# Optimization experiments

Measured on AMD Instinct MI355X. Metric: run time of the kernel, lower is better.

## Reference

```python
import jax, jax.numpy as jnp
import numpy as np

B, C, N = 8, 512, 2048

def setup_inputs() -> dict:
    key = jax.random.key(0)
    ks = jax.random.split(key, 7)
    s = 1.0 / np.sqrt(C)
    return {
        "x": jax.random.normal(ks[0], (B, C, N), dtype=jnp.float32),
        "wq": jax.random.normal(ks[1], (C, C), dtype=jnp.float32) * s,
        "bq": jax.random.normal(ks[2], (C,), dtype=jnp.float32) * s,
        "wk": jax.random.normal(ks[3], (C, C), dtype=jnp.float32) * s,
        "bk": jax.random.normal(ks[4], (C,), dtype=jnp.float32) * s,
        "wv": jax.random.normal(ks[5], (C, C), dtype=jnp.float32) * s,
        "bv": jax.random.normal(ks[6], (C,), dtype=jnp.float32) * s,
    }

def reference(x, wq, bq, wk, bk, wv, bv):
    # Conv1d with kernel=1 == pointwise channel matmul: [B,C,N] -> [B,C,N]
    q = jnp.einsum('oc,bcn->bon', wq, x) + bq[None, :, None]
    k = jnp.einsum('oc,bcn->bon', wk, x) + bk[None, :, None]
    v = jnp.einsum('oc,bcn->bon', wv, x) + bv[None, :, None]
    # scores[b,i,j] = sum_c q[b,c,i] * k[b,c,j]; softmax over j (no scaling, as in source)
    scores = jnp.einsum('bci,bcj->bij', q, k)
    attn = jax.nn.softmax(scores, axis=-1)  # [B,N,N]
    # out[b,c,i] = sum_j v[b,c,j] * attn[b,i,j]
    out = jnp.einsum('bcj,bij->bci', v, attn)
    return out + x
```

## Files before the change

### kernel.cpp

```cpp
#include <hip/hip_runtime.h>
#include <hip/hip_bf16.h>

typedef _Float16 half_t;
typedef _Float16 f16x8 __attribute__((ext_vector_type(8)));
typedef float f32x4 __attribute__((ext_vector_type(4)));

#define AS1 __attribute__((address_space(1)))
#define AS3 __attribute__((address_space(3)))

constexpr int CB = 512;
constexpr int NB = 2048;
constexpr int BB = 8;

__device__ inline f32x4 mfma16(f16x8 a, f16x8 b, f32x4 c) {
  return __builtin_amdgcn_mfma_f32_16x16x32_f16(a, b, c, 0, 0, 0);
}

__device__ inline void xcd_swizzle(int& bx, int& by, int& bz) {
  const int gx = gridDim.x, gy = gridDim.y, gz = gridDim.z;
  const int nwg = gx * gy * gz;
  int lin = blockIdx.x + gx * (blockIdx.y + gy * blockIdx.z);
  if ((nwg & 7) == 0) {
    const int q = nwg >> 3;
    lin = (lin & 7) * q + (lin >> 3);
  }
  bx = lin % gx;
  int tmp = lin / gx;
  by = tmp % gy;
  bz = tmp / gy;
}

__global__ __launch_bounds__(256) void prep_all(
    const float* __restrict__ x, const float* __restrict__ wq,
    const float* __restrict__ wk, const float* __restrict__ wv,
    const float* __restrict__ bq,
    half_t* __restrict__ xh, half_t* __restrict__ xn,
    half_t* __restrict__ wvh, float* __restrict__ u, float* __restrict__ Gp) {
  __shared__ float smem[64 * 68 * 2];
  const int b = blockIdx.x;
  const int t = threadIdx.x;

  if (b < 8192) {
    float (*tile)[33] = (float(*)[33])smem;
    const int bz = b >> 10, by = (b >> 6) & 15, bx = b & 63;
    const int c0 = by * 32, n0 = bx * 32;
    const int tx = t & 31, ty = t >> 5;
    const float* xb = x + (size_t)bz * CB * NB;
    half_t* xnb = xn + (size_t)bz * CB * NB;
#pragma unroll
    for (int r = 0; r < 4; r++) {
      float v = xb[(size_t)(c0 + ty + 8 * r) * NB + n0 + tx];
      tile[ty + 8 * r][tx] = v;
      xnb[(size_t)(c0 + ty + 8 * r) * NB + n0 + tx] = (half_t)v;
    }
    __syncthreads();
    size_t base = (size_t)bz * NB * CB;
#pragma unroll
    for (int r = 0; r < 4; r++)
      xh[base + (size_t)(n0 + ty + 8 * r) * CB + c0 + tx] = (half_t)tile[tx][ty + 8 * r];
  } else if (b < 8704) {
    const int g = b - 8192;
    const int d0 = (g & 7) * 64, c0 = ((g >> 3) & 7) * 64, o0 = (g >> 6) * 64;
    float (*aq)[68] = (float(*)[68])smem;
    float (*ak)[68] = (float(*)[68])(smem + 64 * 68);
    {
      const int r = t >> 2, cbase = (t & 3) * 16;
      const float* q = wq + (size_t)(o0 + r) * CB + c0 + cbase;
      const float* k = wk + (size_t)(o0 + r) * CB + d0 + cbase;
#pragma unroll
      for (int q4 = 0; q4 < 4; q4++) {
        *(float4*)&aq[r][cbase + q4 * 4] = *(const float4*)(q + q4 * 4);
        *(float4*)&ak[r][cbase + q4 * 4] = *(const float4*)(k + q4 * 4);
      }
    }
    __syncthreads();
    const int tc = t & 15, td = t >> 4;
    float acc[4][4] = {};
#pragma unroll 8
    for (int o = 0; o < 64; o++) {
      float4 a4 = *(const float4*)&aq[o][tc * 4];
      float4 b4 = *(const float4*)&ak[o][td * 4];
      float av[4] = {a4.x, a4.y, a4.z, a4.w};
      float bv[4] = {b4.x, b4.y, b4.z, b4.w};
#pragma unroll
      for (int i = 0; i < 4; i++)
#pragma unroll
        for (int j = 0; j < 4; j++)
          acc[i][j] += av[i] * bv[j];
    }
    float* gz = Gp + (size_t)(g >> 6) * CB * CB;
#pragma unroll
    for (int i = 0; i < 4; i++) {
      int c = c0 + tc * 4 + i;
#pragma unroll
      for (int j = 0; j < 4; j++)
        gz[(size_t)c * CB + d0 + td * 4 + j] = acc[i][j];
    }
  } else {
    const int p = b - 8704;
    if (p < 1024) {
      int i = p * 256 + t;
      if (i < CB * CB) wvh[i] = (half_t)wv[i];
    } else {
      int d = (p - 1024) * 256 + t;
      if (d < CB) {
        float s = 0.0f;
        for (int o = 0; o < CB; o++) s += bq[o] * wk[(size_t)o * CB + d];
        u[d] = s;
      }
    }
  }
}

__global__ __launch_bounds__(256) void prep2(
    const float* __restrict__ Gp, half_t* __restrict__ Gh,
    const half_t* __restrict__ xh, const float* __restrict__ u,
    float* __restrict__ ub) {
  const int b = blockIdx.x;
  const int t = threadIdx.x;
  if (b < 1024) {
    int i = b * 256 + t;
    if (i < CB * CB) {
      float s = 0.0f;
#pragma unroll
      for (int z = 0; z < 8; z++) s += Gp[(size_t)z * CB * CB + i];
      Gh[i] = (half_t)s;
    }
  } else {
    __shared__ float us[CB];
    for (int i = t; i < CB; i += 256) us[i] = u[i];
    __syncthreads();
    int row = (b - 1024) * 4 + (t >> 6);
    int lane = t & 63;
    f16x8 vh = *(const f16x8*)(xh + (size_t)row * CB + lane * 8);
    float s = 0.0f;
#pragma unroll
    for (int i = 0; i < 8; i++) s += us[lane * 8 + i] * (float)vh[i];
#pragma unroll
    for (int off = 32; off; off >>= 1) s += __shfl_xor(s, off);
    if (lane == 0) ub[row] = s;
  }
}

__global__ __launch_bounds__(512) void gemm_s256(
    const half_t* __restrict__ xh, const half_t* __restrict__ YTh,
    short* __restrict__ Ss, const float* __restrict__ ub) {
  constexpr int NT = 16;
  constexpr int BUFE = 16384;
  __shared__ alignas(16) half_t sm[3 * BUFE];

  int bxi, byi, bzi;
  xcd_swizzle(bxi, byi, bzi);
  const int t = threadIdx.x;
  const int z = bzi;
  const half_t* Ap = xh  + (size_t)z * NB * CB + (size_t)(byi * 256) * CB;
  const half_t* Bp = YTh + (size_t)z * NB * CB + (size_t)(bxi * 256) * CB;

  const int wid = t >> 6, wm = wid >> 2, wn = wid & 3;
  const int l15 = t & 15, hi = (t >> 4) & 3;
  const int sr = t >> 2, sc = (t & 3) * 8;

  f32x4 acc[8][4] = {};

  auto stageA = [&](int buf, int kt) {
    half_t* dst = sm + buf * BUFE;
#pragma unroll
    for (int i = 0; i < 2; i++)
      __builtin_amdgcn_global_load_lds(
          (const AS1 void*)(Ap + (size_t)(i * 128 + sr) * CB + kt * 32 + sc),
          (AS3 void*)(dst + i * 4096 + t * 8), 16, 0, 0);
  };
  auto stageB = [&](int buf, int kt) {
    half_t* dst = sm + buf * BUFE + 8192;
#pragma unroll
    for (int i = 0; i < 2; i++)
      __builtin_amdgcn_global_load_lds(
          (const AS1 void*)(Bp + (size_t)(i * 128 + sr) * CB + kt * 32 + sc),
          (AS3 void*)(dst + i * 4096 + t * 8), 16, 0, 0);
  };

  stageA(0, 0); stageB(0, 0);
  stageA(1, 1); stageB(1, 1);
  asm volatile("s_waitcnt vmcnt(4)" ::: "memory");
  __builtin_amdgcn_s_barrier();
  asm volatile("" ::: "memory");

  int rb = 0;
  for (int kt = 0; kt < NT; kt++) {
    const half_t* Abuf = sm + rb * BUFE;
    const half_t* Bbuf = Abuf + 8192;
    const int sb = (rb + 2 >= 3) ? rb - 1 : rb + 2;

    f16x8 af[8], bf[4];
#pragma unroll
    for (int f = 0; f < 4; f++)
      af[f] = *(const f16x8*)(Abuf + (wm * 128 + f * 16 + l15) * 32 + hi * 8);
#pragma unroll
    for (int n = 0; n < 4; n++)
      bf[n] = *(const f16x8*)(Bbuf + (wn * 64 + n * 16 + l15) * 32 + hi * 8);
    if (kt + 2 < NT) stageA(sb, kt + 2);
    __builtin_amdgcn_s_barrier();
    asm volatile("s_waitcnt lgkmcnt(0)" ::: "memory");
    __builtin_amdgcn_s_setprio(1);
#pragma unroll
    for (int m = 0; m < 4; m++)
#pragma unroll
      for (int n = 0; n < 4; n++)
        acc[m][n] = mfma16(af[m], bf[n], acc[m][n]);
    __builtin_amdgcn_s_setprio(0);
    __builtin_amdgcn_s_barrier();
    asm volatile("" ::: "memory");

#pragma unroll
    for (int f = 4; f < 8; f++)
      af[f] = *(const f16x8*)(Abuf + (wm * 128 + f * 16 + l15) * 32 + hi * 8);
    if (kt + 2 < NT) stageB(sb, kt + 2);
    __builtin_amdgcn_s_barrier();
    asm volatile("s_waitcnt lgkmcnt(0)" ::: "memory");
    __builtin_amdgcn_s_setprio(1);
#pragma unroll
    for (int m = 4; m < 8; m++)
#pragma unroll
      for (int n = 0; n < 4; n++)
        acc[m][n] = mfma16(af[m], bf[n], acc[m][n]);
    __builtin_amdgcn_s_setprio(0);
    if (kt + 1 < NT) {
      if (kt + 2 < NT) asm volatile("s_waitcnt vmcnt(4)" ::: "memory");
      else             asm volatile("s_waitcnt vmcnt(0)" ::: "memory");
    }
    __builtin_amdgcn_s_barrier();
    asm volatile("" ::: "memory");
    rb = (rb + 1 == 3) ? 0 : rb + 1;
  }

  const int row0 = byi * 256 + wm * 128;
  const int col0 = bxi * 256 + wn * 64;
  short* Sz = Ss + (size_t)z * NB * NB;
  const float* ubz = ub + (size_t)z * NB;
#pragma unroll
  for (int m = 0; m < 8; m++) {
    int rowb = row0 + m * 16 + hi * 4;
#pragma unroll
    for (int n = 0; n < 4; n++) {
      int col = col0 + n * 16 + l15;
      float bc = ubz[col];
#pragma unroll
      for (int r = 0; r < 4; r++) {
        float sv = fminf(fmaxf((acc[m][n][r] + bc) * 256.0f, -32767.0f), 32767.0f);
        Sz[(size_t)(rowb + r) * NB + col] = (short)__float2int_rn(sv);
      }
    }
  }
}

template <int BIAS, int EPI, int NT>
__global__ __launch_bounds__(256) void gemm_nt(
    const half_t* __restrict__ A, int lda, long sA,
    const half_t* __restrict__ Bh, int ldb, long sB,
    void* __restrict__ D, int ldd, long sD,
    const float* __restrict__ bias, long sBias,
    const half_t* __restrict__ R, int ldr, long sR) {
  constexpr int TSZ = 128 * 32;
  __shared__ alignas(16) half_t sm[2 * 2 * TSZ];

  int bxi, byi, bzi;
  xcd_swizzle(bxi, byi, bzi);
  const int t = threadIdx.x;
  const int z = bzi;
  const half_t* Ab  = A  + (size_t)z * sA + (size_t)(byi * 128) * lda;
  const half_t* Bbh = Bh + (size_t)z * sB + (size_t)(bxi * 128) * ldb;
  const int wid = t >> 6, l15 = t & 15, hi = (t >> 4) & 3;
  const int wr = wid >> 1, wc = wid & 1;
  const int lineA = t >> 2, eoff = (t & 3) * 8;

  f32x4 acc[4][4] = {};

  auto stage = [&](int buf, int kt) {
    half_t* base = sm + buf * (2 * TSZ);
#pragma unroll
    for (int p = 0; p < 2; p++) {
      size_t goA = (size_t)(p * 64 + lineA) * lda + kt * 32 + eoff;
      size_t goB = (size_t)(p * 64 + lineA) * ldb + kt * 32 + eoff;
      int lo = p * 2048 + t * 8;
      __builtin_amdgcn_global_load_lds((const AS1 void*)(Ab + goA),  (AS3 void*)(base + lo), 16, 0, 0);
      __builtin_amdgcn_global_load_lds((const AS1 void*)(Bbh + goB), (AS3 void*)(base + TSZ + lo), 16, 0, 0);
    }
  };

  stage(0, 0);
  __syncthreads();
  int cur = 0;
  for (int kt = 0; kt < NT; kt++) {
    if (kt + 1 < NT) stage(cur ^ 1, kt + 1);
    const half_t* bb = sm + cur * (2 * TSZ);
    f16x8 af[4], bf[4];
#pragma unroll
    for (int f = 0; f < 4; f++) {
      af[f] = *(const f16x8*)(bb + (wr * 64 + f * 16 + l15) * 32 + hi * 8);
      bf[f] = *(const f16x8*)(bb + TSZ + (wc * 64 + f * 16 + l15) * 32 + hi * 8);
    }
#pragma unroll
    for (int fm = 0; fm < 4; fm++)
#pragma unroll
      for (int fn = 0; fn < 4; fn++)
        acc[fm][fn] = mfma16(af[fm], bf[fn], acc[fm][fn]);
    __syncthreads();
    cur ^= 1;
  }

  const int row0 = byi * 128 + wr * 64;
  const int col0 = bxi * 128 + wc * 64;
#pragma unroll
  for (int fm = 0; fm < 4; fm++) {
    int rowb = row0 + fm * 16 + hi * 4;
#pragma unroll
    for (int fn = 0; fn < 4; fn++) {
      int col = col0 + fn * 16 + l15;
      float bc = (BIAS == 1) ? bias[(size_t)z * sBias + col] : 0.0f;
#pragma unroll
      for (int r = 0; r < 4; r++) {
        float val = acc[fm][fn][r] + bc;
        size_t di = (size_t)(rowb + r) * ldd + col;
        if (EPI == 3) {
          val += (float)R[(size_t)z * sR + (size_t)(rowb + r) * ldr + col];
          ((float*)D)[(size_t)z * sD + di] = val;
        } else {
          float sv = fminf(fmaxf(val * 256.0f, -32767.0f), 32767.0f);
          ((short*)D)[(size_t)z * sD + di] = (short)__float2int_rn(sv);
        }
      }
    }
  }
}

__global__ __launch_bounds__(256) void gemm_vyt(
    const half_t* __restrict__ xh, const half_t* __restrict__ wvh,
    const half_t* __restrict__ Gh, const float* __restrict__ bv,
    half_t* __restrict__ v, half_t* __restrict__ YTh) {
  constexpr int TSZ = 128 * 32;
  __shared__ alignas(16) half_t sm[2 * 2 * TSZ];

  int bxi, byi, bzi;
  xcd_swizzle(bxi, byi, bzi);
  const int t = threadIdx.x;

  const half_t* Ab;
  const half_t* Bb;
  half_t* Dz;
  int ldd, row0b, col0b;
  const float* rowbias = nullptr;
  if (bzi < 8) {
    const int z = bzi;
    Ab = wvh + (size_t)(byi * 128) * CB;
    Bb = xh + (size_t)z * NB * CB + (size_t)(bxi * 128) * CB;
    Dz = v + (size_t)z * CB * NB;
    ldd = NB; row0b = byi * 128; col0b = bxi * 128;
    rowbias = bv;
  } else {
    const int z = bzi - 8;
    const int lin2 = byi * 16 + bxi;
    const int xp = lin2 & 3, yp = lin2 >> 2;
    Ab = xh + (size_t)z * NB * CB + (size_t)(yp * 128) * CB;
    Bb = Gh + (size_t)(xp * 128) * CB;
    Dz = YTh + (size_t)z * NB * CB;
    ldd = CB; row0b = yp * 128; col0b = xp * 128;
  }

  const int wid = t >> 6, l15 = t & 15, hi = (t >> 4) & 3;
  const int wr = wid >> 1, wc = wid & 1;
  const int lineA = t >> 2, eoff = (t & 3) * 8;

  f32x4 acc[4][4] = {};

  auto stage = [&](int buf, int kt) {
    half_t* base = sm + buf * (2 * TSZ);
#pragma unroll
    for (int p = 0; p < 2; p++) {
      size_t go = (size_t)(p * 64 + lineA) * CB + kt * 32 + eoff;
      int lo = p * 2048 + t * 8;
      __builtin_amdgcn_global_load_lds((const AS1 void*)(Ab + go), (AS3 void*)(base + lo), 16, 0, 0);
      __builtin_amdgcn_global_load_lds((const AS1 void*)(Bb + go), (AS3 void*)(base + TSZ + lo), 16, 0, 0);
    }
  };

  stage(0, 0);
  __syncthreads();
  int cur = 0;
  for (int kt = 0; kt < 16; kt++) {
    if (kt + 1 < 16) stage(cur ^ 1, kt + 1);
    const half_t* bb = sm + cur * (2 * TSZ);
    f16x8 af[4], bf[4];
#pragma unroll
    for (int f = 0; f < 4; f++) {
      af[f] = *(const f16x8*)(bb + (wr * 64 + f * 16 + l15) * 32 + hi * 8);
      bf[f] = *(const f16x8*)(bb + TSZ + (wc * 64 + f * 16 + l15) * 32 + hi * 8);
    }
#pragma unroll
    for (int fm = 0; fm < 4; fm++)
#pragma unroll
      for (int fn = 0; fn < 4; fn++)
        acc[fm][fn] = mfma16(af[fm], bf[fn], acc[fm][fn]);
    __syncthreads();
    cur ^= 1;
  }

  const int row0 = row0b + wr * 64;
  const int col0 = col0b + wc * 64;
#pragma unroll
  for (int fm = 0; fm < 4; fm++) {
    int rowb = row0 + fm * 16 + hi * 4;
#pragma unroll
    for (int fn = 0; fn < 4; fn++) {
      int col = col0 + fn * 16 + l15;
#pragma unroll
      for (int r = 0; r < 4; r++) {
        float val = acc[fm][fn][r];
        if (rowbias) val += rowbias[rowb + r];
        Dz[(size_t)(rowb + r) * ldd + col] = (half_t)val;
      }
    }
  }
}

struct alignas(16) H8 { half_t h[8]; };
struct alignas(16) S8 { short s[8]; };

__global__ __launch_bounds__(256) void softmax_rows(const short* __restrict__ S,
                                                    half_t* __restrict__ P) {
  const short* row = S + (size_t)blockIdx.x * NB;
  int t = threadIdx.x;
  S8 r8 = *reinterpret_cast<const S8*>(row + t * 8);
  float vals[8];
#pragma unroll
  for (int i = 0; i < 8; i++) vals[i] = (float)r8.s[i] * 0.00390625f;
  float m = vals[0];
#pragma unroll
  for (int i = 1; i < 8; i++) m = fmaxf(m, vals[i]);
#pragma unroll
  for (int off = 32; off; off >>= 1) m = fmaxf(m, __shfl_xor(m, off));
  __shared__ float redm[4], reds[4];
  if ((t & 63) == 0) redm[t >> 6] = m;
  __syncthreads();
  m = fmaxf(fmaxf(redm[0], redm[1]), fmaxf(redm[2], redm[3]));
  float e[8], s = 0.0f;
#pragma unroll
  for (int i = 0; i < 8; i++) { e[i] = __expf(vals[i] - m); s += e[i]; }
#pragma unroll
  for (int off = 32; off; off >>= 1) s += __shfl_xor(s, off);
  if ((t & 63) == 0) reds[t >> 6] = s;
  __syncthreads();
  s = reds[0] + reds[1] + reds[2] + reds[3];
  float inv = 1.0f / s;
  H8 ob;
#pragma unroll
  for (int i = 0; i < 8; i++) ob.h[i] = (half_t)(e[i] * inv);
  *reinterpret_cast<H8*>(P + (size_t)blockIdx.x * NB + t * 8) = ob;
}

extern "C" void kernel_launch(void* const* d_in, const int* in_sizes, int n_in,
                              void* d_out, int out_size, void* d_ws, size_t ws_size,
                              hipStream_t stream) {
  const float* x  = (const float*)d_in[0];
  const float* wq = (const float*)d_in[1];
  const float* bq = (const float*)d_in[2];
  const float* wk = (const float*)d_in[3];
  const float* wv = (const float*)d_in[5];
  const float* bv = (const float*)d_in[6];
  float* out = (float*)d_out;

  const size_t MB = 1u << 20;
  if (ws_size < 196 * MB) return;

  char* ws = (char*)d_ws;
  half_t* xh   = (half_t*)(ws + 0);
  half_t* YTh  = (half_t*)(ws + 16 * MB);
  half_t* v    = (half_t*)(ws + 32 * MB);
  short*  Ss   = (short*)(ws + 48 * MB);
  float*  Gp   = (float*)(ws + 48 * MB);
  half_t* Pd   = (half_t*)(ws + 112 * MB);
  half_t* xn   = (half_t*)(ws + 176 * MB);
  half_t* Gh   = (half_t*)(ws + 192 * MB);
  half_t* wvh  = (half_t*)(ws + 192 * MB + 512 * 1024);
  float*  u    = (float*)(ws + 193 * MB);
  float*  ub   = (float*)(ws + 193 * MB + 256 * 1024);

  prep_all<<<9730, 256, 0, stream>>>(x, wq, wk, wv, bq, xh, xn, wvh, u, Gp);
  prep2<<<5120, 256, 0, stream>>>(Gp, Gh, xh, u, ub);

  gemm_vyt<<<dim3(16, 4, 16), 256, 0, stream>>>(xh, wvh, Gh, bv, v, YTh);

  gemm_s256<<<dim3(8, 8, 8), 512, 0, stream>>>(xh, YTh, Ss, ub);

  softmax_rows<<<BB * NB, 256, 0, stream>>>(Ss, Pd);

  gemm_nt<0, 3, 64><<<dim3(16, 4, 8), 256, 0, stream>>>(
      v, NB, (long)CB * NB,
      Pd, NB, (long)NB * NB,
      out, NB, (long)CB * NB, nullptr, 0,
      xn, NB, (long)CB * NB);
}
```

Measured before the change: 194.8 us.

## Replace PV GEMM with 128x256-tile, 512-thread, triple-buffered pipelined kernel

Replaces the generic 128x128, 256-thread double-buffered NT GEMM used for the V·P^T output stage with a dedicated kernel. The new kernel uses 128x256 tiles with 8 waves, a 64-deep K step split into two 32-wide substeps, and a three-buffer LDS ring with explicit vmcnt waits, barriers and raised MFMA priority. The aim is more reuse of each loaded tile and better overlap of global-to-LDS loads with MFMA work. In exchange it uses more LDS and launches half as many workgroups (256), which can lower occupancy and leave part of the device idle.

```diff
diff --git a/kernel.cpp b/kernel.cpp
--- a/kernel.cpp
+++ b/kernel.cpp
@@ -253,82 +253,93 @@
   }
 }
 
-template <int BIAS, int EPI, int NT>
-__global__ __launch_bounds__(256) void gemm_nt(
-    const half_t* __restrict__ A, int lda, long sA,
-    const half_t* __restrict__ Bh, int ldb, long sB,
-    void* __restrict__ D, int ldd, long sD,
-    const float* __restrict__ bias, long sBias,
-    const half_t* __restrict__ R, int ldr, long sR) {
-  constexpr int TSZ = 128 * 32;
-  __shared__ alignas(16) half_t sm[2 * 2 * TSZ];
+__global__ __launch_bounds__(512) void gemm_pv256(
+    const half_t* __restrict__ V, const half_t* __restrict__ Pd,
+    const half_t* __restrict__ xn, float* __restrict__ out) {
+  constexpr int NSUP = 32;
+  constexpr int BUFE = 24576;
+  __shared__ alignas(16) half_t sm[3 * BUFE];
 
   int bxi, byi, bzi;
   xcd_swizzle(bxi, byi, bzi);
-  const int t = threadIdx.x;
-  const int z = bzi;
-  const half_t* Ab  = A  + (size_t)z * sA + (size_t)(byi * 128) * lda;
-  const half_t* Bbh = Bh + (size_t)z * sB + (size_t)(bxi * 128) * ldb;
-  const int wid = t >> 6, l15 = t & 15, hi = (t >> 4) & 3;
-  const int wr = wid >> 1, wc = wid & 1;
-  const int lineA = t >> 2, eoff = (t & 3) * 8;
+  const int t = threadIdx.x, z = bzi;
+  const half_t* Ap = V  + (size_t)z * CB * NB + (size_t)(byi * 128) * NB;
+  const half_t* Bp = Pd + (size_t)z * NB * NB + (size_t)(bxi * 256) * NB;
+
+  const int wid = t >> 6, wm = wid >> 2, wn = wid & 3;
+  const int l15 = t & 15, hi = (t >> 4) & 3;
+  const int sr = t >> 2, sc = (t & 3) * 8;
 
   f32x4 acc[4][4] = {};
 
-  auto stage = [&](int buf, int kt) {
-    half_t* base = sm + buf * (2 * TSZ);
-#pragma unroll
-    for (int p = 0; p < 2; p++) {
-      size_t goA = (size_t)(p * 64 + lineA) * lda + kt * 32 + eoff;
-      size_t goB = (size_t)(p * 64 + lineA) * ldb + kt * 32 + eoff;
-      int lo = p * 2048 + t * 8;
-      __builtin_amdgcn_global_load_lds((const AS1 void*)(Ab + goA),  (AS3 void*)(base + lo), 16, 0, 0);
-      __builtin_amdgcn_global_load_lds((const AS1 void*)(Bbh + goB), (AS3 void*)(base + TSZ + lo), 16, 0, 0);
-    }
+  auto stageA = [&](int buf, int u, int ks) {
+    __builtin_amdgcn_global_load_lds(
+        (const AS1 void*)(Ap + (size_t)sr * NB + u * 64 + ks * 32 + sc),
+        (AS3 void*)(sm + buf * BUFE + ks * 4096 + t * 8), 16, 0, 0);
   };
-
-  stage(0, 0);
-  __syncthreads();
-  int cur = 0;
-  for (int kt = 0; kt < NT; kt++) {
-    if (kt + 1 < NT) stage(cur ^ 1, kt + 1);
-    const half_t* bb = sm + cur * (2 * TSZ);
-    f16x8 af[4], bf[4];
-#pragma unroll
-    for (int f = 0; f < 4; f++) {
-      af[f] = *(const f16x8*)(bb + (wr * 64 + f * 16 + l15) * 32 + hi * 8);
-      bf[f] = *(const f16x8*)(bb + TSZ + (wc * 64 + f * 16 + l15) * 32 + hi * 8);
-    }
-#pragma unroll
-    for (int fm = 0; fm < 4; fm++)
-#pragma unroll
-      for (int fn = 0; fn < 4; fn++)
-        acc[fm][fn] = mfma16(af[fm], bf[fn], acc[fm][fn]);
-    __syncthreads();
-    cur ^= 1;
-  }
-
-  const int row0 = byi * 128 + wr * 64;
-  const int col0 = bxi * 128 + wc * 64;
-#pragma unroll
-  for (int fm = 0; fm < 4; fm++) {
-    int rowb = row0 + fm * 16 + hi * 4;
-#pragma unroll
-    for (int fn = 0; fn < 4; fn++) {
-      int col = col0 + fn * 16 + l15;
-      float bc = (BIAS == 1) ? bias[(size_t)z * sBias + col] : 0.0f;
-#pragma unroll
-      for (int r = 0; r < 4; r++) {
-        float val = acc[fm][fn][r] + bc;
-        size_t di = (size_t)(rowb + r) * ldd + col;
-        if (EPI == 3) {
-          val += (float)R[(size_t)z * sR + (size_t)(rowb + r) * ldr + col];
-          ((float*)D)[(size_t)z * sD + di] = val;
-        } else {
-          float sv = fminf(fmaxf(val * 256.0f, -32767.0f), 32767.0f);
-          ((short*)D)[(size_t)z * sD + di] = (short)__float2int_rn(sv);
-        }
+  auto stageB = [&](int buf, int u, int ks) {
+    half_t* dst = sm + buf * BUFE + 8192 + ks * 8192;
+#pragma unroll
+    for (int p = 0; p < 2; p++)
+      __builtin_amdgcn_global_load_lds(
+          (const AS1 void*)(Bp + (size_t)(p * 128 + sr) * NB + u * 64 + ks * 32 + sc),
+          (AS3 void*)(dst + p * 4096 + t * 8), 16, 0, 0);
+  };
+
+  stageA(0, 0, 0); stageB(0, 0, 0); stageA(0, 0, 1); stageB(0, 0, 1);
+  stageA(1, 1, 0); stageB(1, 1, 0); stageA(1, 1, 1); stageB(1, 1, 1);
+  asm volatile("s_waitcnt vmcnt(6)" ::: "memory");
+  __builtin_amdgcn_s_barrier();
+  asm volatile("" ::: "memory");
+
+  int rb = 0;
+  for (int u = 0; u < NSUP; u++) {
+    const half_t* Abuf = sm + rb * BUFE;
+    const half_t* Bbuf = Abuf + 8192;
+    const int sb = (rb + 2 >= 3) ? rb - 1 : rb + 2;
+#pragma unroll
+    for (int ks = 0; ks < 2; ks++) {
+      f16x8 af[4], bf[4];
+#pragma unroll
+      for (int f = 0; f < 4; f++)
+        af[f] = *(const f16x8*)(Abuf + ks * 4096 + (wm * 64 + f * 16 + l15) * 32 + hi * 8);
+#pragma unroll
+      for (int n = 0; n < 4; n++)
+        bf[n] = *(const f16x8*)(Bbuf + ks * 8192 + (wn * 64 + n * 16 + l15) * 32 + hi * 8);
+      if (u + 2 < NSUP) { stageA(sb, u + 2, ks); stageB(sb, u + 2, ks); }
+      __builtin_amdgcn_s_barrier();
+      asm volatile("s_waitcnt lgkmcnt(0)" ::: "memory");
+      __builtin_amdgcn_s_setprio(1);
+#pragma unroll
+      for (int m = 0; m < 4; m++)
+#pragma unroll
+        for (int n = 0; n < 4; n++)
+          acc[m][n] = mfma16(af[m], bf[n], acc[m][n]);
+      __builtin_amdgcn_s_setprio(0);
+      if (ks == 1 && u + 1 < NSUP) {
+        if (u + 2 < NSUP) asm volatile("s_waitcnt vmcnt(6)" ::: "memory");
+        else              asm volatile("s_waitcnt vmcnt(0)" ::: "memory");
       }
+      __builtin_amdgcn_s_barrier();
+      asm volatile("" ::: "memory");
+    }
+    rb = (rb + 1 == 3) ? 0 : rb + 1;
+  }
+
+  const int row0 = byi * 128 + wm * 64;
+  const int col0 = bxi * 256 + wn * 64;
+  float* Oz = out + (size_t)z * CB * NB;
+  const half_t* Rz = xn + (size_t)z * CB * NB;
+#pragma unroll
+  for (int m = 0; m < 4; m++) {
+    int rowb = row0 + m * 16 + hi * 4;
+#pragma unroll
+    for (int n = 0; n < 4; n++) {
+      int col = col0 + n * 16 + l15;
+#pragma unroll
+      for (int r = 0; r < 4; r++)
+        Oz[(size_t)(rowb + r) * NB + col] =
+            acc[m][n][r] + (float)Rz[(size_t)(rowb + r) * NB + col];
     }
   }
 }
@@ -493,9 +504,5 @@
 
   softmax_rows<<<BB * NB, 256, 0, stream>>>(Ss, Pd);
 
-  gemm_nt<0, 3, 64><<<dim3(16, 4, 8), 256, 0, stream>>>(
-      v, NB, (long)CB * NB,
-      Pd, NB, (long)NB * NB,
-      out, NB, (long)CB * NB, nullptr, 0,
-      xn, NB, (long)CB * NB);
-}
+  gemm_pv256<<<dim3(8, 4, 8), 512, 0, stream>>>(v, Pd, xn, out);
+}
```

Result: faster. 189.1 us (median of 3 runs) (-2.9%).
